# Performance work log

Hardware: AMD Instinct MI355X
Metric: run time of the kernel (lower is better)

## Reference

```python
import jax, jax.numpy as jnp
import numpy as np

N_TEXT = 90000
N_NON = 10000
N = N_TEXT + N_NON
E = 500000
EMB = 256
NREL = 500
ROUNDS = 2
RROUNDS = 2
NUM_SAMPLES = 5
PRED_IN = 4 * EMB + 2 * 2 + 2 * 2 * (ROUNDS + RROUNDS)  # 1044


def setup_inputs() -> dict:
    key = jax.random.key(0)
    ks = jax.random.split(key, 16)
    inp = {
        "h_id_tensor": jax.random.randint(ks[0], (E,), 0, N, dtype=jnp.int64),
        "r_id_tensor": jax.random.randint(ks[1], (E,), 0, NREL, dtype=jnp.int64),
        "t_id_tensor": jax.random.randint(ks[2], (E,), 0, N, dtype=jnp.int64),
        "q_emb": jax.random.normal(ks[3], (1, EMB), dtype=jnp.float32),
        "entity_embs": jax.random.normal(ks[4], (N_TEXT, EMB), dtype=jnp.float32),
        "num_non_text_entities": N_NON,
        "relation_embs": jax.random.normal(ks[5], (NREL, EMB), dtype=jnp.float32),
        "topic_entity_one_hot": jax.random.uniform(ks[6], (N, 2), dtype=jnp.float32),
        # learned parameters
        "non_text_emb": jax.random.normal(ks[7], (1, EMB), dtype=jnp.float32) * 0.02,
        "w1_mu": jax.random.normal(ks[8], (EMB, PRED_IN), dtype=jnp.float32) * 0.2,
        "w1_rho": -3.0 + 0.1 * jax.random.normal(ks[9], (EMB, PRED_IN), dtype=jnp.float32),
        "b1_mu": jax.random.normal(ks[10], (EMB,), dtype=jnp.float32) * 0.2,
        "b1_rho": -3.0 + 0.1 * jax.random.normal(ks[11], (EMB,), dtype=jnp.float32),
        "w2_mu": jax.random.normal(ks[12], (1, EMB), dtype=jnp.float32) * 0.2,
        "w2_rho": -3.0 + 0.1 * jax.random.normal(ks[13], (1, EMB), dtype=jnp.float32),
        "b2_mu": jax.random.normal(ks[14], (1,), dtype=jnp.float32) * 0.2,
        "b2_rho": -3.0 + 0.1 * jax.random.normal(ks[15], (1,), dtype=jnp.float32),
    }
    return inp


def _peconv_mean(src, dst, x, n):
    # PyG MessagePassing(aggr='mean'): mean of x[src] grouped by dst; 0 for isolated nodes
    s = jax.ops.segment_sum(x[src], dst, num_segments=n)
    c = jax.ops.segment_sum(jnp.ones((src.shape[0], 1), x.dtype), dst, num_segments=n)
    return s / jnp.maximum(c, 1.0)


def reference(h_id_tensor, r_id_tensor, t_id_tensor, q_emb, entity_embs,
              num_non_text_entities, relation_embs, topic_entity_one_hot,
              non_text_emb, w1_mu, w1_rho, b1_mu, b1_rho, w2_mu, w2_rho, b2_mu, b2_rho):
    n = topic_entity_one_hot.shape[0]
    # entity features: text embeddings + shared non-text embedding rows
    h_e0 = jnp.concatenate(
        [entity_embs, jnp.broadcast_to(non_text_emb, (num_non_text_entities, non_text_emb.shape[-1]))], axis=0)
    feats = [h_e0, topic_entity_one_hot]
    # DDE forward rounds: edge_index = (h -> t)
    h = topic_entity_one_hot
    for _ in range(ROUNDS):
        h = _peconv_mean(h_id_tensor, t_id_tensor, h, n)
        feats.append(h)
    # DDE reverse rounds: edge_index = (t -> h)
    h = topic_entity_one_hot
    for _ in range(RROUNDS):
        h = _peconv_mean(t_id_tensor, h_id_tensor, h, n)
        feats.append(h)
    h_e = jnp.concatenate(feats, axis=1)  # [N, PRED_IN//2 - ...]
    h_r = relation_embs[r_id_tensor]      # [E, EMB]
    h_q = jnp.broadcast_to(q_emb, (h_r.shape[0], q_emb.shape[-1]))
    h_triple = jnp.concatenate([h_q, h_e[h_id_tensor], h_r, h_e[t_id_tensor]], axis=1)  # [E, 1044]
    # Bayesian MLP: NUM_SAMPLES reparameterized samples, averaged
    key = jax.random.key(42)
    w1_sig = jax.nn.softplus(w1_rho)
    b1_sig = jax.nn.softplus(b1_rho)
    w2_sig = jax.nn.softplus(w2_rho)
    b2_sig = jax.nn.softplus(b2_rho)
    outs = []
    for i in range(NUM_SAMPLES):
        sk = jax.random.split(jax.random.fold_in(key, i), 4)
        w1 = w1_mu + jax.random.normal(sk[0], w1_mu.shape, w1_mu.dtype) * w1_sig
        b1 = b1_mu + jax.random.normal(sk[1], b1_mu.shape, b1_mu.dtype) * b1_sig
        w2 = w2_mu + jax.random.normal(sk[2], w2_mu.shape, w2_mu.dtype) * w2_sig
        b2 = b2_mu + jax.random.normal(sk[3], b2_mu.shape, b2_mu.dtype) * b2_sig
        h1 = jax.nn.relu(h_triple @ w1.T + b1)
        outs.append(h1 @ w2.T + b2)
    return jnp.mean(jnp.stack(outs), axis=0)  # [E, 1]
```

## Files before the change

kernel.cpp:

```cpp
#include <hip/hip_runtime.h>
#include <hip/hip_bf16.h>

typedef __attribute__((ext_vector_type(8))) short short8;
typedef __attribute__((ext_vector_type(4))) float f32x4;
typedef unsigned long long u64;

#define GLOAD16(g, l) __builtin_amdgcn_global_load_lds( \
    (const __attribute__((address_space(1))) void*)(g), \
    (__attribute__((address_space(3))) void*)(l), 16, 0, 0)

#define F18 262144.0f
#define F18I (1.0f / 262144.0f)
#define F20 1048576.0f
#define F20I (1.0f / 1048576.0f)

#define TF_ROUND(r) { x0 += x1; x1 = ((x1<<(r))|(x1>>(32-(r)))); x1 ^= x0; }

__device__ __forceinline__ void tf2x32(unsigned k0, unsigned k1, unsigned x0, unsigned x1,
                                       unsigned &o0, unsigned &o1)
{
  unsigned ks2 = k0 ^ k1 ^ 0x1BD11BDAu;
  x0 += k0; x1 += k1;
  TF_ROUND(13) TF_ROUND(15) TF_ROUND(26) TF_ROUND(6)
  x0 += k1;  x1 += ks2 + 1u;
  TF_ROUND(17) TF_ROUND(29) TF_ROUND(16) TF_ROUND(24)
  x0 += ks2; x1 += k0 + 2u;
  TF_ROUND(13) TF_ROUND(15) TF_ROUND(26) TF_ROUND(6)
  x0 += k0;  x1 += k1 + 3u;
  TF_ROUND(17) TF_ROUND(29) TF_ROUND(16) TF_ROUND(24)
  x0 += k1;  x1 += ks2 + 4u;
  TF_ROUND(13) TF_ROUND(15) TF_ROUND(26) TF_ROUND(6)
  x0 += ks2; x1 += k0 + 5u;
  o0 = x0; o1 = x1;
}

__device__ __forceinline__ float erfinv_f(float x)
{
  float w = -log1pf(-x * x);
  float p;
  if (w < 5.0f) {
    w -= 2.5f;
    p = 2.81022636e-08f;
    p = fmaf(p, w, 3.43273939e-07f);
    p = fmaf(p, w, -3.5233877e-06f);
    p = fmaf(p, w, -4.39150654e-06f);
    p = fmaf(p, w, 0.00021858087f);
    p = fmaf(p, w, -0.00125372503f);
    p = fmaf(p, w, -0.00417768164f);
    p = fmaf(p, w, 0.246640727f);
    p = fmaf(p, w, 1.50140941f);
  } else {
    w = sqrtf(w) - 3.0f;
    p = -0.000200214257f;
    p = fmaf(p, w, 0.000100950558f);
    p = fmaf(p, w, 0.00134934322f);
    p = fmaf(p, w, -0.00367342844f);
    p = fmaf(p, w, 0.00573950773f);
    p = fmaf(p, w, -0.0076224613f);
    p = fmaf(p, w, 0.00943887047f);
    p = fmaf(p, w, 1.00167406f);
    p = fmaf(p, w, 2.83297682f);
  }
  return p * x;
}

__device__ __forceinline__ float rng_normal(unsigned b)
{
  float f = __uint_as_float((b >> 9) | 0x3f800000u) - 1.0f;
  const float lo = -0.99999994f;
  float u = fmaxf(lo, f * 2.0f + lo);
  return 1.41421356f * erfinv_f(u);
}

__device__ __forceinline__ float softplusf(float x) { return log1pf(expf(x)); }

__global__ void dde_pass1(const int* __restrict__ h, const int* __restrict__ t,
                          const float* __restrict__ topic,
                          u64* __restrict__ P1t, u64* __restrict__ P1h, int E)
{
  int e = blockIdx.x * blockDim.x + threadIdx.x;
  if (e >= E) return;
  int hh = h[e], tt = t[e];
  float2 th = *reinterpret_cast<const float2*>(&topic[hh * 2]);
  float2 tv = *reinterpret_cast<const float2*>(&topic[tt * 2]);
  u64 vt = (1ULL << 52) | ((u64)(unsigned)(th.y * F18 + 0.5f) << 26) | (unsigned)(th.x * F18 + 0.5f);
  u64 vh = (1ULL << 52) | ((u64)(unsigned)(tv.y * F18 + 0.5f) << 26) | (unsigned)(tv.x * F18 + 0.5f);
  atomicAdd(&P1t[tt], vt);
  atomicAdd(&P1h[hh], vh);
}

__global__ void dde_norm1(const u64* __restrict__ P1t, const u64* __restrict__ P1h,
                          float* __restrict__ f1n, float* __restrict__ g1n, int N)
{
  int n = blockIdx.x * blockDim.x + threadIdx.x;
  if (n >= N) return;
  u64 pt = P1t[n];
  float st = F18I / fmaxf((float)(unsigned)(pt >> 52), 1.0f);
  f1n[n*2+0] = (float)(unsigned)(pt & 0x3FFFFFFu) * st;
  f1n[n*2+1] = (float)(unsigned)((pt >> 26) & 0x3FFFFFFu) * st;
  u64 ph = P1h[n];
  float sh = F18I / fmaxf((float)(unsigned)(ph >> 52), 1.0f);
  g1n[n*2+0] = (float)(unsigned)(ph & 0x3FFFFFFu) * sh;
  g1n[n*2+1] = (float)(unsigned)((ph >> 26) & 0x3FFFFFFu) * sh;
}

__global__ void dde_pass2(const int* __restrict__ h, const int* __restrict__ t,
                          const float* __restrict__ f1n, const float* __restrict__ g1n,
                          u64* __restrict__ F2_t, u64* __restrict__ G2_h, int E)
{
  int e = blockIdx.x * blockDim.x + threadIdx.x;
  if (e >= E) return;
  int hh = h[e], tt = t[e];
  float2 fv = *reinterpret_cast<const float2*>(&f1n[hh * 2]);
  float2 gv = *reinterpret_cast<const float2*>(&g1n[tt * 2]);
  atomicAdd(&F2_t[tt], ((u64)(unsigned)(fv.y * F20 + 0.5f) << 32) | (unsigned)(fv.x * F20 + 0.5f));
  atomicAdd(&G2_h[hh], ((u64)(unsigned)(gv.y * F20 + 0.5f) << 32) | (unsigned)(gv.x * F20 + 0.5f));
}

__global__ void dde_norm2(const u64* __restrict__ F2_t, const u64* __restrict__ G2_h,
                          const u64* __restrict__ P1t, const u64* __restrict__ P1h,
                          float* __restrict__ f2n, float* __restrict__ g2n, int N)
{
  int n = blockIdx.x * blockDim.x + threadIdx.x;
  if (n >= N) return;
  float st = F20I / fmaxf((float)(unsigned)(P1t[n] >> 52), 1.0f);
  u64 f = F2_t[n];
  f2n[n*2+0] = (float)(unsigned)(f & 0xFFFFFFFFu) * st;
  f2n[n*2+1] = (float)(unsigned)(f >> 32) * st;
  float sh = F20I / fmaxf((float)(unsigned)(P1h[n] >> 52), 1.0f);
  u64 g = G2_h[n];
  g2n[n*2+0] = (float)(unsigned)(g & 0xFFFFFFFFu) * sh;
  g2n[n*2+1] = (float)(unsigned)(g >> 32) * sh;
}

__global__ void build_he(const float* __restrict__ emb, const float* __restrict__ nte,
                         const float* __restrict__ topic,
                         const float* __restrict__ f1, const float* __restrict__ f2,
                         const float* __restrict__ g1, const float* __restrict__ g2,
                         __hip_bfloat16* __restrict__ He, int N, int nText)
{
  int idx = blockIdx.x * blockDim.x + threadIdx.x;
  if (idx >= N * 288) return;
  int n = idx / 288, j = idx - n * 288;
  float v;
  if (j < 256)      v = (n < nText) ? emb[(size_t)n*256 + j] : nte[j];
  else if (j < 258) v = topic[n*2 + (j-256)];
  else if (j < 260) v = f1[n*2 + (j-258)];
  else if (j < 262) v = f2[n*2 + (j-260)];
  else if (j < 264) v = g1[n*2 + (j-262)];
  else if (j < 266) v = g2[n*2 + (j-264)];
  else              v = 0.0f;
  He[idx] = __float2bfloat16(v);
}

__global__ void rel_cvt(const float* __restrict__ rel, __hip_bfloat16* __restrict__ relb, int n)
{
  int i = blockIdx.x * blockDim.x + threadIdx.x;
  if (i < n) relb[i] = __float2bfloat16(rel[i]);
}

__global__ void sample_kernel(int s,
                              const float* __restrict__ w1_mu, const float* __restrict__ w1_rho,
                              const float* __restrict__ b1_mu, const float* __restrict__ b1_rho,
                              const float* __restrict__ w2_mu, const float* __restrict__ w2_rho,
                              const float* __restrict__ b2_mu, const float* __restrict__ b2_rho,
                              float* __restrict__ W1s, float* __restrict__ b1s,
                              float* __restrict__ w2s, float* __restrict__ b2s,
                              __hip_bfloat16* __restrict__ As, __hip_bfloat16* __restrict__ Asr)
{
  const int W1N = 267264;
  int tid = blockIdx.x * blockDim.x + threadIdx.x;
  unsigned F0, F1;
  tf2x32(0u, 42u, 0u, (unsigned)s, F0, F1);

  if (tid < W1N) {
    unsigned k0, k1; tf2x32(F0, F1, 0u, 0u, k0, k1);
    unsigned o0, o1; tf2x32(k0, k1, 0u, (unsigned)tid, o0, o1);
    float w = fmaf(rng_normal(o0 ^ o1), softplusf(w1_rho[tid]), w1_mu[tid]);
    W1s[tid] = w;
    int m = tid / 1044, j = tid - m * 1044;
    if (j >= 256 && j < 522)      As[m * 288 + (j - 256)]         = __float2bfloat16(w);
    else if (j >= 522 && j < 778) Asr[m * 256 + (j - 522)]        = __float2bfloat16(w);
    else if (j >= 778)            As[(256 + m) * 288 + (j - 778)] = __float2bfloat16(w);
  } else if (tid < W1N + 256) {
    int m = tid - W1N;
    unsigned k0, k1; tf2x32(F0, F1, 0u, 1u, k0, k1);
    unsigned o0, o1; tf2x32(k0, k1, 0u, (unsigned)m, o0, o1);
    b1s[m] = fmaf(rng_normal(o0 ^ o1), softplusf(b1_rho[m]), b1_mu[m]);
  } else if (tid < W1N + 512) {
    int m = tid - (W1N + 256);
    unsigned k0, k1; tf2x32(F0, F1, 0u, 2u, k0, k1);
    unsigned o0, o1; tf2x32(k0, k1, 0u, (unsigned)m, o0, o1);
    w2s[m] = fmaf(rng_normal(o0 ^ o1), softplusf(w2_rho[m]), w2_mu[m]);
  } else if (tid == W1N + 512) {
    unsigned k0, k1; tf2x32(F0, F1, 0u, 3u, k0, k1);
    unsigned o0, o1; tf2x32(k0, k1, 0u, 0u, o0, o1);
    b2s[0] = fmaf(rng_normal(o0 ^ o1), softplusf(b2_rho[0]), b2_mu[0]);
  }
}

__global__ void c_kernel(const float* __restrict__ W1s, const float* __restrict__ b1s,
                         const float* __restrict__ q, float* __restrict__ cvec)
{
  int k = blockIdx.x * 4 + (threadIdx.x >> 6);
  int lane = threadIdx.x & 63;
  float4 v  = *reinterpret_cast<const float4*>(&W1s[(size_t)k * 1044 + lane * 4]);
  float4 qv = *reinterpret_cast<const float4*>(&q[lane * 4]);
  float acc = v.x*qv.x + v.y*qv.y + v.z*qv.z + v.w*qv.w;
  #pragma unroll
  for (int off = 32; off >= 1; off >>= 1) acc += __shfl_down(acc, off, 64);
  if (lane == 0) cvec[k] = acc + b1s[k];
}

__global__ __launch_bounds__(256) void ar_mfma(const __hip_bfloat16* __restrict__ relb_,
                                               const __hip_bfloat16* __restrict__ Asr_,
                                               __hip_bfloat16* __restrict__ Arb, int NRr)
{
  const int lane = threadIdx.x & 63;
  const int wid  = threadIdx.x >> 6;
  const int wr = wid >> 1, wc = wid & 1;
  const int r0 = blockIdx.y * 128 + wr * 64;
  const int k0 = blockIdx.x * 128 + wc * 64;
  const int lr = lane & 15, lk = (lane >> 4) * 8;
  const short* A = (const short*)relb_;
  const short* B = (const short*)Asr_;

  const short* pa[4];
  const short* pb[4];
  #pragma unroll
  for (int i = 0; i < 4; ++i) {
    int rr = r0 + i * 16 + lr; if (rr >= NRr) rr = NRr - 1;
    pa[i] = A + (size_t)rr * 256 + lk;
    pb[i] = B + (size_t)(k0 + i * 16 + lr) * 256 + lk;
  }
  f32x4 acc[4][4] = {};
  #pragma unroll
  for (int ks = 0; ks < 8; ++ks) {
    short8 a[4], b[4];
    #pragma unroll
    for (int i = 0; i < 4; ++i) a[i] = *reinterpret_cast<const short8*>(pa[i] + ks * 32);
    #pragma unroll
    for (int j = 0; j < 4; ++j) b[j] = *reinterpret_cast<const short8*>(pb[j] + ks * 32);
    #pragma unroll
    for (int i = 0; i < 4; ++i)
      #pragma unroll
      for (int j = 0; j < 4; ++j)
        acc[i][j] = __builtin_amdgcn_mfma_f32_16x16x32_bf16(a[i], b[j], acc[i][j], 0, 0, 0);
  }
  const int rg = (lane >> 4) * 4;
  #pragma unroll
  for (int i = 0; i < 4; ++i) {
    #pragma unroll
    for (int r_ = 0; r_ < 4; ++r_) {
      int r = r0 + i * 16 + rg + r_;
      if (r < NRr) {
        #pragma unroll
        for (int j = 0; j < 4; ++j)
          Arb[(size_t)r * 256 + k0 + j * 16 + lr] = __float2bfloat16(acc[i][j][r_]);
      }
    }
  }
}

__global__ __launch_bounds__(256) void gemm_mfma(const __hip_bfloat16* __restrict__ Heb,
                                                 const __hip_bfloat16* __restrict__ Asb,
                                                 __hip_bfloat16* __restrict__ U, int nEnt)
{
  __shared__ short lA[2][4096];
  __shared__ short lB[2][4096];

  const int tid  = threadIdx.x;
  const int lane = tid & 63;
  const int wid  = tid >> 6;
  const int wr   = wid >> 1;
  const int wc   = wid & 1;
  const int m0   = blockIdx.x * 128;
  const int n0   = blockIdx.y * 128;
  const short* He = (const short*)Heb;
  const short* As = (const short*)Asb;

  const int lr  = lane & 15;
  const int kb  = (lane >> 4) * 16;
  const int swz = (lane & 3) << 4;

  const int g0row = tid >> 2,  g0c = tid & 3;
  const int g1row = (tid + 256) >> 2;
  const int maxA = nEnt - n0 - 1;
  const int a0r = g0row <= maxA ? g0row : maxA;
  const int a1r = g1row <= maxA ? g1row : maxA;
  const size_t aoff0 = (size_t)a0r * 288 + (g0c ^ (g0row & 3)) * 8;
  const size_t aoff1 = (size_t)a1r * 288 + (g0c ^ (g1row & 3)) * 8;
  const size_t boff0 = (size_t)g0row * 288 + (g0c ^ (g0row & 3)) * 8;
  const size_t boff1 = (size_t)g1row * 288 + (g0c ^ (g1row & 3)) * 8;
  const short* gA = He + (size_t)n0 * 288;
  const short* gB = As + (size_t)m0 * 288;

  #define STAGE(buf, k0)                                              \
    { GLOAD16(gA + (k0) + aoff0, (char*)lA[buf] + tid * 16);          \
      GLOAD16(gA + (k0) + aoff1, (char*)lA[buf] + tid * 16 + 4096);   \
      GLOAD16(gB + (k0) + boff0, (char*)lB[buf] + tid * 16);          \
      GLOAD16(gB + (k0) + boff1, (char*)lB[buf] + tid * 16 + 4096); }

  f32x4 acc[4][4] = {};

  STAGE(0, 0)
  __syncthreads();

  #pragma unroll 1
  for (int ks = 0; ks < 9; ++ks) {
    const int cur = ks & 1;
    if (ks < 8) STAGE(cur ^ 1, (ks + 1) * 32)

    short8 a[4], b[4];
    #pragma unroll
    for (int i = 0; i < 4; ++i) {
      int rowA = wr * 64 + i * 16 + lr;
      a[i] = *reinterpret_cast<const short8*>((const char*)lA[cur] + rowA * 64 + (kb ^ swz));
      int rowB = wc * 64 + i * 16 + lr;
      b[i] = *reinterpret_cast<const short8*>((const char*)lB[cur] + rowB * 64 + (kb ^ swz));
    }
    #pragma unroll
    for (int i = 0; i < 4; ++i)
      #pragma unroll
      for (int j = 0; j < 4; ++j)
        acc[i][j] = __builtin_amdgcn_mfma_f32_16x16x32_bf16(a[i], b[j], acc[i][j], 0, 0, 0);

    __syncthreads();
  }
  #undef STAGE

  const int rg = (lane >> 4) * 4;
  #pragma unroll
  for (int i = 0; i < 4; ++i) {
    #pragma unroll
    for (int r = 0; r < 4; ++r) {
      int n = n0 + wr * 64 + i * 16 + rg + r;
      if (n < nEnt) {
        #pragma unroll
        for (int j = 0; j < 4; ++j)
          U[(size_t)n * 512 + m0 + wc * 64 + j * 16 + lr] = __float2bfloat16(acc[i][j][r]);
      }
    }
  }
}

__global__ __launch_bounds__(256) void edge_kernel(const int* __restrict__ h,
                                                   const int* __restrict__ t,
                                                   const int* __restrict__ r,
                                                   const __hip_bfloat16* __restrict__ U,
                                                   const __hip_bfloat16* __restrict__ Arb,
                                                   const float* __restrict__ cvec,
                                                   const float* __restrict__ w2s,
                                                   const float* __restrict__ b2s,
                                                   float* __restrict__ out, int E, int mode)
{
  int e = blockIdx.x * 8 + (threadIdx.x >> 5);
  int l = threadIdx.x & 31;
  if (e >= E) return;
  int hh = h[e], tt = t[e], rr = r[e];
  const ushort* Ub = (const ushort*)U;
  const ushort* Ab = (const ushort*)Arb;

  uint4 uhv = *reinterpret_cast<const uint4*>(Ub + (size_t)hh * 512 + l * 8);
  uint4 utv = *reinterpret_cast<const uint4*>(Ub + (size_t)tt * 512 + 256 + l * 8);
  uint4 arv = *reinterpret_cast<const uint4*>(Ab + (size_t)rr * 256 + l * 8);
  float4 c0  = *reinterpret_cast<const float4*>(&cvec[l * 8]);
  float4 c1  = *reinterpret_cast<const float4*>(&cvec[l * 8 + 4]);
  float4 w0  = *reinterpret_cast<const float4*>(&w2s[l * 8]);
  float4 w1  = *reinterpret_cast<const float4*>(&w2s[l * 8 + 4]);

  float uh[8], ut[8], aa[8];
  uh[0] = __uint_as_float(uhv.x << 16); uh[1] = __uint_as_float(uhv.x & 0xFFFF0000u);
  uh[2] = __uint_as_float(uhv.y << 16); uh[3] = __uint_as_float(uhv.y & 0xFFFF0000u);
  uh[4] = __uint_as_float(uhv.z << 16); uh[5] = __uint_as_float(uhv.z & 0xFFFF0000u);
  uh[6] = __uint_as_float(uhv.w << 16); uh[7] = __uint_as_float(uhv.w & 0xFFFF0000u);
  ut[0] = __uint_as_float(utv.x << 16); ut[1] = __uint_as_float(utv.x & 0xFFFF0000u);
  ut[2] = __uint_as_float(utv.y << 16); ut[3] = __uint_as_float(utv.y & 0xFFFF0000u);
  ut[4] = __uint_as_float(utv.z << 16); ut[5] = __uint_as_float(utv.z & 0xFFFF0000u);
  ut[6] = __uint_as_float(utv.w << 16); ut[7] = __uint_as_float(utv.w & 0xFFFF0000u);
  aa[0] = __uint_as_float(arv.x << 16); aa[1] = __uint_as_float(arv.x & 0xFFFF0000u);
  aa[2] = __uint_as_float(arv.y << 16); aa[3] = __uint_as_float(arv.y & 0xFFFF0000u);
  aa[4] = __uint_as_float(arv.z << 16); aa[5] = __uint_as_float(arv.z & 0xFFFF0000u);
  aa[6] = __uint_as_float(arv.w << 16); aa[7] = __uint_as_float(arv.w & 0xFFFF0000u);

  const float cc[8] = {c0.x, c0.y, c0.z, c0.w, c1.x, c1.y, c1.z, c1.w};
  const float ww[8] = {w0.x, w0.y, w0.z, w0.w, w1.x, w1.y, w1.z, w1.w};

  float sum = 0.0f;
  #pragma unroll
  for (int i = 0; i < 8; ++i)
    sum += ww[i] * fmaxf(cc[i] + uh[i] + aa[i] + ut[i], 0.0f);

  #pragma unroll
  for (int off = 16; off >= 1; off >>= 1) sum += __shfl_down(sum, off, 32);

  if (l == 0) {
    float v = sum + b2s[0];
    if (mode == 0)      out[e] = v;
    else if (mode == 1) out[e] += v;
    else                out[e] = (out[e] + v) * 0.2f;
  }
}

extern "C" void kernel_launch(void* const* d_in, const int* in_sizes, int n_in,
                              void* d_out, int out_size, void* d_ws, size_t ws_size,
                              hipStream_t stream)
{
  const int*   h_id  = (const int*)  d_in[0];
  const int*   r_id  = (const int*)  d_in[1];
  const int*   t_id  = (const int*)  d_in[2];
  const float* q     = (const float*)d_in[3];
  const float* emb   = (const float*)d_in[4];
  const float* rel   = (const float*)d_in[6];
  const float* topic = (const float*)d_in[7];
  const float* nte   = (const float*)d_in[8];
  const float* w1_mu = (const float*)d_in[9];
  const float* w1_rho= (const float*)d_in[10];
  const float* b1_mu = (const float*)d_in[11];
  const float* b1_rho= (const float*)d_in[12];
  const float* w2_mu = (const float*)d_in[13];
  const float* w2_rho= (const float*)d_in[14];
  const float* b2_mu = (const float*)d_in[15];
  const float* b2_rho= (const float*)d_in[16];

  const int E     = in_sizes[0];
  const int nText = in_sizes[4] / 256;
  const int N     = in_sizes[7] / 2;
  const int NR    = in_sizes[6] / 256;
  float* out = (float*)d_out;

  char* ws = (char*)d_ws;
  size_t off = 0;
  auto alloc = [&](size_t bytes) -> void* {
    void* p = (void*)(ws + off);
    off += (bytes + 255) & ~(size_t)255;
    return p;
  };
  __hip_bfloat16* He  = (__hip_bfloat16*)alloc((size_t)N * 288 * 2);
  __hip_bfloat16* U   = (__hip_bfloat16*)alloc((size_t)N * 512 * 2);
  __hip_bfloat16* Asr = (__hip_bfloat16*)alloc(256 * 256 * 2);
  __hip_bfloat16* relb= (__hip_bfloat16*)alloc((size_t)NR * 256 * 2);
  __hip_bfloat16* Arb = (__hip_bfloat16*)alloc((size_t)NR * 256 * 2);
  float* W1s  = (float*)alloc(267264 * 4);
  float* b1s  = (float*)alloc(256 * 4);
  float* w2s  = (float*)alloc(256 * 4);
  float* b2s  = (float*)alloc(64 * 4);
  float* cvec = (float*)alloc(256 * 4);
  float* f1n  = (float*)alloc((size_t)2 * N * 4);
  float* f2n  = (float*)alloc((size_t)2 * N * 4);
  float* g1n  = (float*)alloc((size_t)2 * N * 4);
  float* g2n  = (float*)alloc((size_t)2 * N * 4);
  __hip_bfloat16* As = (__hip_bfloat16*)alloc(512 * 288 * 2);
  u64* P1t  = (u64*)alloc((size_t)N * 8);
  u64* P1h  = (u64*)alloc((size_t)N * 8);
  u64* F2_t = (u64*)alloc((size_t)N * 8);
  u64* G2_h = (u64*)alloc((size_t)N * 8);

  size_t zero_bytes = (size_t)((char*)(G2_h + N) - (char*)As);
  hipMemsetAsync(As, 0, zero_bytes, stream);

  int eb = (E + 255) / 256;
  int nb = (N + 255) / 256;
  dde_pass1<<<eb, 256, 0, stream>>>(h_id, t_id, topic, P1t, P1h, E);
  dde_norm1<<<nb, 256, 0, stream>>>(P1t, P1h, f1n, g1n, N);
  dde_pass2<<<eb, 256, 0, stream>>>(h_id, t_id, f1n, g1n, F2_t, G2_h, E);
  dde_norm2<<<nb, 256, 0, stream>>>(F2_t, G2_h, P1t, P1h, f2n, g2n, N);

  int heb = ((int)((size_t)N * 288) + 255) / 256;
  build_he<<<heb, 256, 0, stream>>>(emb, nte, topic, f1n, f2n, g1n, g2n, He, N, nText);
  rel_cvt<<<(NR * 256 + 255) / 256, 256, 0, stream>>>(rel, relb, NR * 256);

  dim3 ggrid(4, (N + 127) / 128);
  dim3 agrid(2, (NR + 127) / 128);
  for (int s = 0; s < 5; ++s) {
    sample_kernel<<<(267264 + 513 + 255) / 256, 256, 0, stream>>>(
        s, w1_mu, w1_rho, b1_mu, b1_rho, w2_mu, w2_rho, b2_mu, b2_rho,
        W1s, b1s, w2s, b2s, As, Asr);
    c_kernel<<<64, 256, 0, stream>>>(W1s, b1s, q, cvec);
    ar_mfma <<<agrid, 256, 0, stream>>>(relb, Asr, Arb, NR);
    gemm_mfma<<<ggrid, 256, 0, stream>>>(He, As, U, N);
    int mode = (s == 0) ? 0 : ((s == 4) ? 2 : 1);
    edge_kernel<<<(E + 7) / 8, 256, 0, stream>>>(h_id, t_id, r_id, U, Arb, cvec,
                                                 w2s, b2s, out, E, mode);
  }
  (void)n_in; (void)out_size; (void)ws_size;
}
```

Before: 970.8 us.

## Split GEMM and edge scoring into two hidden-dimension halves per sample

```diff
diff --git a/kernel.cpp b/kernel.cpp
--- a/kernel.cpp
+++ b/kernel.cpp
@@ -264,7 +264,8 @@
 
 __global__ __launch_bounds__(256) void gemm_mfma(const __hip_bfloat16* __restrict__ Heb,
                                                  const __hip_bfloat16* __restrict__ Asb,
-                                                 __hip_bfloat16* __restrict__ U, int nEnt)
+                                                 __hip_bfloat16* __restrict__ U, int nEnt,
+                                                 int mbase)
 {
   __shared__ short lA[2][4096];
   __shared__ short lB[2][4096];
@@ -274,7 +275,7 @@
   const int wid  = tid >> 6;
   const int wr   = wid >> 1;
   const int wc   = wid & 1;
-  const int m0   = blockIdx.x * 128;
+  const int m0   = mbase + blockIdx.x * 256;
   const int n0   = blockIdx.y * 128;
   const short* He = (const short*)Heb;
   const short* As = (const short*)Asb;
@@ -344,15 +345,16 @@
   }
 }
 
-__global__ __launch_bounds__(256) void edge_kernel(const int* __restrict__ h,
-                                                   const int* __restrict__ t,
-                                                   const int* __restrict__ r,
-                                                   const __hip_bfloat16* __restrict__ U,
-                                                   const __hip_bfloat16* __restrict__ Arb,
-                                                   const float* __restrict__ cvec,
-                                                   const float* __restrict__ w2s,
-                                                   const float* __restrict__ b2s,
-                                                   float* __restrict__ out, int E, int mode)
+__global__ __launch_bounds__(256) void edge_half(const int* __restrict__ h,
+                                                 const int* __restrict__ t,
+                                                 const int* __restrict__ r,
+                                                 const __hip_bfloat16* __restrict__ U,
+                                                 const __hip_bfloat16* __restrict__ Arb,
+                                                 const float* __restrict__ cvec,
+                                                 const float* __restrict__ w2s,
+                                                 const float* __restrict__ b2s,
+                                                 float* __restrict__ out, int E,
+                                                 int half, int mode)
 {
   int e = blockIdx.x * 8 + (threadIdx.x >> 5);
   int l = threadIdx.x & 31;
@@ -360,45 +362,38 @@
   int hh = h[e], tt = t[e], rr = r[e];
   const ushort* Ub = (const ushort*)U;
   const ushort* Ab = (const ushort*)Arb;
-
-  uint4 uhv = *reinterpret_cast<const uint4*>(Ub + (size_t)hh * 512 + l * 8);
-  uint4 utv = *reinterpret_cast<const uint4*>(Ub + (size_t)tt * 512 + 256 + l * 8);
-  uint4 arv = *reinterpret_cast<const uint4*>(Ab + (size_t)rr * 256 + l * 8);
-  float4 c0  = *reinterpret_cast<const float4*>(&cvec[l * 8]);
-  float4 c1  = *reinterpret_cast<const float4*>(&cvec[l * 8 + 4]);
-  float4 w0  = *reinterpret_cast<const float4*>(&w2s[l * 8]);
-  float4 w1  = *reinterpret_cast<const float4*>(&w2s[l * 8 + 4]);
-
-  float uh[8], ut[8], aa[8];
+  const int kb = half * 128 + l * 4;
+
+  uint2 uhv = *reinterpret_cast<const uint2*>(Ub + (size_t)hh * 512 + kb);
+  uint2 utv = *reinterpret_cast<const uint2*>(Ub + (size_t)tt * 512 + 256 + kb);
+  uint2 arv = *reinterpret_cast<const uint2*>(Ab + (size_t)rr * 256 + kb);
+  float4 cc = *reinterpret_cast<const float4*>(&cvec[kb]);
+  float4 ww = *reinterpret_cast<const float4*>(&w2s[kb]);
+
+  float uh[4], ut[4], aa[4];
   uh[0] = __uint_as_float(uhv.x << 16); uh[1] = __uint_as_float(uhv.x & 0xFFFF0000u);
   uh[2] = __uint_as_float(uhv.y << 16); uh[3] = __uint_as_float(uhv.y & 0xFFFF0000u);
-  uh[4] = __uint_as_float(uhv.z << 16); uh[5] = __uint_as_float(uhv.z & 0xFFFF0000u);
-  uh[6] = __uint_as_float(uhv.w << 16); uh[7] = __uint_as_float(uhv.w & 0xFFFF0000u);
   ut[0] = __uint_as_float(utv.x << 16); ut[1] = __uint_as_float(utv.x & 0xFFFF0000u);
   ut[2] = __uint_as_float(utv.y << 16); ut[3] = __uint_as_float(utv.y & 0xFFFF0000u);
-  ut[4] = __uint_as_float(utv.z << 16); ut[5] = __uint_as_float(utv.z & 0xFFFF0000u);
-  ut[6] = __uint_as_float(utv.w << 16); ut[7] = __uint_as_float(utv.w & 0xFFFF0000u);
   aa[0] = __uint_as_float(arv.x << 16); aa[1] = __uint_as_float(arv.x & 0xFFFF0000u);
   aa[2] = __uint_as_float(arv.y << 16); aa[3] = __uint_as_float(arv.y & 0xFFFF0000u);
-  aa[4] = __uint_as_float(arv.z << 16); aa[5] = __uint_as_float(arv.z & 0xFFFF0000u);
-  aa[6] = __uint_as_float(arv.w << 16); aa[7] = __uint_as_float(arv.w & 0xFFFF0000u);
-
-  const float cc[8] = {c0.x, c0.y, c0.z, c0.w, c1.x, c1.y, c1.z, c1.w};
-  const float ww[8] = {w0.x, w0.y, w0.z, w0.w, w1.x, w1.y, w1.z, w1.w};
+
+  const float c4[4] = {cc.x, cc.y, cc.z, cc.w};
+  const float w4[4] = {ww.x, ww.y, ww.z, ww.w};
 
   float sum = 0.0f;
   #pragma unroll
-  for (int i = 0; i < 8; ++i)
-    sum += ww[i] * fmaxf(cc[i] + uh[i] + aa[i] + ut[i], 0.0f);
+  for (int i = 0; i < 4; ++i)
+    sum += w4[i] * fmaxf(c4[i] + uh[i] + aa[i] + ut[i], 0.0f);
 
   #pragma unroll
   for (int off = 16; off >= 1; off >>= 1) sum += __shfl_down(sum, off, 32);
 
   if (l == 0) {
-    float v = sum + b2s[0];
-    if (mode == 0)      out[e] = v;
-    else if (mode == 1) out[e] += v;
-    else                out[e] = (out[e] + v) * 0.2f;
+    if (half) sum += b2s[0];
+    if (mode == 0)      out[e] = sum;
+    else if (mode == 1) out[e] += sum;
+    else                out[e] = (out[e] + sum) * 0.2f;
   }
 }
 
@@ -470,18 +465,21 @@
   build_he<<<heb, 256, 0, stream>>>(emb, nte, topic, f1n, f2n, g1n, g2n, He, N, nText);
   rel_cvt<<<(NR * 256 + 255) / 256, 256, 0, stream>>>(rel, relb, NR * 256);
 
-  dim3 ggrid(4, (N + 127) / 128);
+  dim3 ggrid(2, (N + 127) / 128);
   dim3 agrid(2, (NR + 127) / 128);
+  int edgeb = (E + 7) / 8;
   for (int s = 0; s < 5; ++s) {
     sample_kernel<<<(267264 + 513 + 255) / 256, 256, 0, stream>>>(
         s, w1_mu, w1_rho, b1_mu, b1_rho, w2_mu, w2_rho, b2_mu, b2_rho,
         W1s, b1s, w2s, b2s, As, Asr);
     c_kernel<<<64, 256, 0, stream>>>(W1s, b1s, q, cvec);
     ar_mfma <<<agrid, 256, 0, stream>>>(relb, Asr, Arb, NR);
-    gemm_mfma<<<ggrid, 256, 0, stream>>>(He, As, U, N);
-    int mode = (s == 0) ? 0 : ((s == 4) ? 2 : 1);
-    edge_kernel<<<(E + 7) / 8, 256, 0, stream>>>(h_id, t_id, r_id, U, Arb, cvec,
-                                                 w2s, b2s, out, E, mode);
+    gemm_mfma<<<ggrid, 256, 0, stream>>>(He, As, U, N, 0);
+    edge_half<<<edgeb, 256, 0, stream>>>(h_id, t_id, r_id, U, Arb, cvec, w2s, b2s,
+                                         out, E, 0, (s == 0) ? 0 : 1);
+    gemm_mfma<<<ggrid, 256, 0, stream>>>(He, As, U, N, 128);
+    edge_half<<<edgeb, 256, 0, stream>>>(h_id, t_id, r_id, U, Arb, cvec, w2s, b2s,
+                                         out, E, 1, (s == 4) ? 2 : 1);
   }
   (void)n_in; (void)out_size; (void)ws_size;
 }
```

New measurement: 1.257 ms. +29.5%, slower.

## Sort edges by head node via counting sort and vectorize He build

Applied to the files above, without the earlier changes.

```diff
diff --git a/kernel.cpp b/kernel.cpp
--- a/kernel.cpp
+++ b/kernel.cpp
@@ -13,6 +13,12 @@
 #define F18I (1.0f / 262144.0f)
 #define F20 1048576.0f
 #define F20I (1.0f / 1048576.0f)
+
+__device__ __forceinline__ ushort f2bf(float v)
+{
+  __hip_bfloat16 b = __float2bfloat16(v);
+  return *reinterpret_cast<ushort*>(&b);
+}
 
 #define TF_ROUND(r) { x0 += x1; x1 = ((x1<<(r))|(x1>>(32-(r)))); x1 ^= x0; }
 
@@ -76,7 +82,8 @@
 
 __global__ void dde_pass1(const int* __restrict__ h, const int* __restrict__ t,
                           const float* __restrict__ topic,
-                          u64* __restrict__ P1t, u64* __restrict__ P1h, int E)
+                          u64* __restrict__ P1t, u64* __restrict__ P1h,
+                          int* __restrict__ hist, int E)
 {
   int e = blockIdx.x * blockDim.x + threadIdx.x;
   if (e >= E) return;
@@ -87,6 +94,7 @@
   u64 vh = (1ULL << 52) | ((u64)(unsigned)(tv.y * F18 + 0.5f) << 26) | (unsigned)(tv.x * F18 + 0.5f);
   atomicAdd(&P1t[tt], vt);
   atomicAdd(&P1h[hh], vh);
+  atomicAdd(&hist[hh], 1);
 }
 
 __global__ void dde_norm1(const u64* __restrict__ P1t, const u64* __restrict__ P1h,
@@ -133,6 +141,74 @@
   g2n[n*2+1] = (float)(unsigned)(g >> 32) * sh;
 }
 
+__global__ void scan1(const int* __restrict__ cnt, int* __restrict__ bsum, int N)
+{
+  __shared__ int sh[256];
+  int b = blockIdx.x, t = threadIdx.x;
+  int base = b * 1024 + t * 4;
+  int s = 0;
+  #pragma unroll
+  for (int i = 0; i < 4; ++i) if (base + i < N) s += cnt[base + i];
+  sh[t] = s;
+  __syncthreads();
+  for (int off = 128; off >= 1; off >>= 1) {
+    if (t < off) sh[t] += sh[t + off];
+    __syncthreads();
+  }
+  if (t == 0) bsum[b] = sh[0];
+}
+
+__global__ void scan2(const int* __restrict__ bsum, int* __restrict__ bscan, int NB)
+{
+  __shared__ int sh[256];
+  int t = threadIdx.x;
+  sh[t] = (t < NB) ? bsum[t] : 0;
+  __syncthreads();
+  if (t == 0) {
+    int run = 0;
+    for (int i = 0; i < NB; ++i) { int v = sh[i]; sh[i] = run; run += v; }
+  }
+  __syncthreads();
+  if (t < NB) bscan[t] = sh[t];
+}
+
+__global__ void scan3(const int* __restrict__ cnt, const int* __restrict__ bscan,
+                      int* __restrict__ cursor, int N)
+{
+  __shared__ int sh[256];
+  int b = blockIdx.x, t = threadIdx.x;
+  int base = b * 1024 + t * 4;
+  int c[4];
+  #pragma unroll
+  for (int i = 0; i < 4; ++i) c[i] = (base + i < N) ? cnt[base + i] : 0;
+  int mysum = c[0] + c[1] + c[2] + c[3];
+  sh[t] = mysum;
+  __syncthreads();
+  for (int off = 1; off < 256; off <<= 1) {
+    int u = (t >= off) ? sh[t - off] : 0;
+    __syncthreads();
+    sh[t] += u;
+    __syncthreads();
+  }
+  int excl = sh[t] - mysum + bscan[b];
+  #pragma unroll
+  for (int i = 0; i < 4; ++i) {
+    if (base + i < N) cursor[base + i] = excl;
+    excl += c[i];
+  }
+}
+
+__global__ void edge_scatter(const int* __restrict__ h, const int* __restrict__ t,
+                             const int* __restrict__ r, int* __restrict__ cursor,
+                             int4* __restrict__ se, int E)
+{
+  int e = blockIdx.x * blockDim.x + threadIdx.x;
+  if (e >= E) return;
+  int hh = h[e];
+  int pos = atomicAdd(&cursor[hh], 1);
+  se[pos] = make_int4(hh, t[e], r[e], e);
+}
+
 __global__ void build_he(const float* __restrict__ emb, const float* __restrict__ nte,
                          const float* __restrict__ topic,
                          const float* __restrict__ f1, const float* __restrict__ f2,
@@ -140,17 +216,36 @@
                          __hip_bfloat16* __restrict__ He, int N, int nText)
 {
   int idx = blockIdx.x * blockDim.x + threadIdx.x;
-  if (idx >= N * 288) return;
-  int n = idx / 288, j = idx - n * 288;
-  float v;
-  if (j < 256)      v = (n < nText) ? emb[(size_t)n*256 + j] : nte[j];
-  else if (j < 258) v = topic[n*2 + (j-256)];
-  else if (j < 260) v = f1[n*2 + (j-258)];
-  else if (j < 262) v = f2[n*2 + (j-260)];
-  else if (j < 264) v = g1[n*2 + (j-262)];
-  else if (j < 266) v = g2[n*2 + (j-264)];
-  else              v = 0.0f;
-  He[idx] = __float2bfloat16(v);
+  if (idx >= N * 36) return;
+  int n = idx / 36, j8 = idx - n * 36;
+  ushort r[8];
+  if (j8 < 32) {
+    const float* src = (n < nText) ? &emb[(size_t)n * 256 + j8 * 8] : &nte[j8 * 8];
+    float4 v0 = *reinterpret_cast<const float4*>(src);
+    float4 v1 = *reinterpret_cast<const float4*>(src + 4);
+    const float vv[8] = {v0.x, v0.y, v0.z, v0.w, v1.x, v1.y, v1.z, v1.w};
+    #pragma unroll
+    for (int i = 0; i < 8; ++i) r[i] = f2bf(vv[i]);
+  } else if (j8 == 32) {
+    float2 tp = *reinterpret_cast<const float2*>(&topic[n*2]);
+    float2 a  = *reinterpret_cast<const float2*>(&f1[n*2]);
+    float2 bq = *reinterpret_cast<const float2*>(&f2[n*2]);
+    float2 cq = *reinterpret_cast<const float2*>(&g1[n*2]);
+    const float vv[8] = {tp.x, tp.y, a.x, a.y, bq.x, bq.y, cq.x, cq.y};
+    #pragma unroll
+    for (int i = 0; i < 8; ++i) r[i] = f2bf(vv[i]);
+  } else if (j8 == 33) {
+    float2 d = *reinterpret_cast<const float2*>(&g2[n*2]);
+    r[0] = f2bf(d.x);
+    r[1] = f2bf(d.y);
+    #pragma unroll
+    for (int i = 2; i < 8; ++i) r[i] = 0;
+  } else {
+    #pragma unroll
+    for (int i = 0; i < 8; ++i) r[i] = 0;
+  }
+  *reinterpret_cast<short8*>((ushort*)He + (size_t)n * 288 + j8 * 8) =
+      *reinterpret_cast<const short8*>(r);
 }
 
 __global__ void rel_cvt(const float* __restrict__ rel, __hip_bfloat16* __restrict__ relb, int n)
@@ -344,26 +439,25 @@
   }
 }
 
-__global__ __launch_bounds__(256) void edge_kernel(const int* __restrict__ h,
-                                                   const int* __restrict__ t,
-                                                   const int* __restrict__ r,
+__global__ __launch_bounds__(256) void edge_kernel(const int4* __restrict__ se,
                                                    const __hip_bfloat16* __restrict__ U,
                                                    const __hip_bfloat16* __restrict__ Arb,
                                                    const float* __restrict__ cvec,
                                                    const float* __restrict__ w2s,
                                                    const float* __restrict__ b2s,
+                                                   float* __restrict__ acc,
                                                    float* __restrict__ out, int E, int mode)
 {
   int e = blockIdx.x * 8 + (threadIdx.x >> 5);
   int l = threadIdx.x & 31;
   if (e >= E) return;
-  int hh = h[e], tt = t[e], rr = r[e];
+  int4 ed = se[e];
   const ushort* Ub = (const ushort*)U;
   const ushort* Ab = (const ushort*)Arb;
 
-  uint4 uhv = *reinterpret_cast<const uint4*>(Ub + (size_t)hh * 512 + l * 8);
-  uint4 utv = *reinterpret_cast<const uint4*>(Ub + (size_t)tt * 512 + 256 + l * 8);
-  uint4 arv = *reinterpret_cast<const uint4*>(Ab + (size_t)rr * 256 + l * 8);
+  uint4 uhv = *reinterpret_cast<const uint4*>(Ub + (size_t)ed.x * 512 + l * 8);
+  uint4 utv = *reinterpret_cast<const uint4*>(Ub + (size_t)ed.y * 512 + 256 + l * 8);
+  uint4 arv = *reinterpret_cast<const uint4*>(Ab + (size_t)ed.z * 256 + l * 8);
   float4 c0  = *reinterpret_cast<const float4*>(&cvec[l * 8]);
   float4 c1  = *reinterpret_cast<const float4*>(&cvec[l * 8 + 4]);
   float4 w0  = *reinterpret_cast<const float4*>(&w2s[l * 8]);
@@ -396,9 +490,9 @@
 
   if (l == 0) {
     float v = sum + b2s[0];
-    if (mode == 0)      out[e] = v;
-    else if (mode == 1) out[e] += v;
-    else                out[e] = (out[e] + v) * 0.2f;
+    if (mode == 0)      acc[e] = v;
+    else if (mode == 1) acc[e] += v;
+    else                out[ed.w] = (acc[e] + v) * 0.2f;
   }
 }
 
@@ -450,28 +544,41 @@
   float* f2n  = (float*)alloc((size_t)2 * N * 4);
   float* g1n  = (float*)alloc((size_t)2 * N * 4);
   float* g2n  = (float*)alloc((size_t)2 * N * 4);
+  float* eacc = (float*)alloc((size_t)E * 4);
+  int4*  se   = (int4*)alloc((size_t)E * 16);
+  const int NB = (N + 1023) / 1024;
+  int* cursor = (int*)alloc((size_t)NB * 1024 * 4);
+  int* bsum   = (int*)alloc(256 * 4);
+  int* bscan  = (int*)alloc(256 * 4);
   __hip_bfloat16* As = (__hip_bfloat16*)alloc(512 * 288 * 2);
   u64* P1t  = (u64*)alloc((size_t)N * 8);
   u64* P1h  = (u64*)alloc((size_t)N * 8);
   u64* F2_t = (u64*)alloc((size_t)N * 8);
   u64* G2_h = (u64*)alloc((size_t)N * 8);
-
-  size_t zero_bytes = (size_t)((char*)(G2_h + N) - (char*)As);
+  int* hist = (int*)alloc((size_t)N * 4);
+
+  size_t zero_bytes = (size_t)((char*)(hist + N) - (char*)As);
   hipMemsetAsync(As, 0, zero_bytes, stream);
 
   int eb = (E + 255) / 256;
   int nb = (N + 255) / 256;
-  dde_pass1<<<eb, 256, 0, stream>>>(h_id, t_id, topic, P1t, P1h, E);
+  dde_pass1<<<eb, 256, 0, stream>>>(h_id, t_id, topic, P1t, P1h, hist, E);
   dde_norm1<<<nb, 256, 0, stream>>>(P1t, P1h, f1n, g1n, N);
   dde_pass2<<<eb, 256, 0, stream>>>(h_id, t_id, f1n, g1n, F2_t, G2_h, E);
   dde_norm2<<<nb, 256, 0, stream>>>(F2_t, G2_h, P1t, P1h, f2n, g2n, N);
 
-  int heb = ((int)((size_t)N * 288) + 255) / 256;
+  scan1<<<NB, 256, 0, stream>>>(hist, bsum, N);
+  scan2<<<1, 256, 0, stream>>>(bsum, bscan, NB);
+  scan3<<<NB, 256, 0, stream>>>(hist, bscan, cursor, N);
+  edge_scatter<<<eb, 256, 0, stream>>>(h_id, t_id, r_id, cursor, se, E);
+
+  int heb = (N * 36 + 255) / 256;
   build_he<<<heb, 256, 0, stream>>>(emb, nte, topic, f1n, f2n, g1n, g2n, He, N, nText);
   rel_cvt<<<(NR * 256 + 255) / 256, 256, 0, stream>>>(rel, relb, NR * 256);
 
   dim3 ggrid(4, (N + 127) / 128);
   dim3 agrid(2, (NR + 127) / 128);
+  int edgeb = (E + 7) / 8;
   for (int s = 0; s < 5; ++s) {
     sample_kernel<<<(267264 + 513 + 255) / 256, 256, 0, stream>>>(
         s, w1_mu, w1_rho, b1_mu, b1_rho, w2_mu, w2_rho, b2_mu, b2_rho,
@@ -480,8 +587,8 @@
     ar_mfma <<<agrid, 256, 0, stream>>>(relb, Asr, Arb, NR);
     gemm_mfma<<<ggrid, 256, 0, stream>>>(He, As, U, N);
     int mode = (s == 0) ? 0 : ((s == 4) ? 2 : 1);
-    edge_kernel<<<(E + 7) / 8, 256, 0, stream>>>(h_id, t_id, r_id, U, Arb, cvec,
-                                                 w2s, b2s, out, E, mode);
+    edge_kernel<<<edgeb, 256, 0, stream>>>(se, U, Arb, cvec, w2s, b2s,
+                                           eacc, out, E, mode);
   }
   (void)n_in; (void)out_size; (void)ws_size;
 }
```

After: 958.9 us. No clear change (-1.2%).
